# Optimization experiments

Hardware: AMD Instinct MI355X
Metric: run time of the kernel (lower is better)

Reference implementation:

```python
import jax, jax.numpy as jnp
import numpy as np

EPS = 1e-6

def oneplus(x):
    return 1.0 + jnp.log1p(jnp.exp(x) + EPS)

def content_addr(mem, keys, strength):
    # mem [B,N,M], keys [B,R,M], strength [B,R] -> [B,R,N]
    mn = jnp.sqrt(jnp.sum(mem * mem, -1))    # [B,N]
    kn = jnp.sqrt(jnp.sum(keys * keys, -1))  # [B,R]
    sim = jnp.einsum('brm,bnm->brn', keys, mem) / (kn[..., None] * mn[:, None, :] + EPS)
    return jax.nn.softmax(strength[..., None] * sim, axis=-1)

def setup_inputs() -> dict:
    key = jax.random.key(0)
    ks = jax.random.split(key, 16)
    B, T, W, R, N, M = 16, 32, 128, 4, 512, 128
    def lin(k, fi, fo):
        k1, k2 = jax.random.split(k)
        s = 1.0 / np.sqrt(fi)
        return (jax.random.uniform(k1, (fi, fo), minval=-s, maxval=s),
                jax.random.uniform(k2, (fo,), minval=-s, maxval=s))
    Din = W + R * W  # controller input: cat(x_t, prev_reads)
    Wb, bb = lin(ks[0], Din + W, W)     # CfC backbone (1 layer, silu)
    Wff1, bff1 = lin(ks[1], W, W)
    Wff2, bff2 = lin(ks[2], W, W)
    Wta, bta = lin(ks[3], W, W)
    Wtb, btb = lin(ks[4], W, W)
    Wv, bv = lin(ks[5], W, W)
    Wr, br = lin(ks[6], W * R, W)
    Wxi, bxi = lin(ks[7], W, W * R + 3 * W + 5 * R + 3)
    X = jax.random.normal(ks[8], (B, T, W), dtype=jnp.float32)
    hs = jnp.zeros((B, W), dtype=jnp.float32)
    mem = jax.random.normal(ks[9], (B, N, M), dtype=jnp.float32) * 0.1
    reset_idxs = jax.random.randint(ks[10], (B, T), 0, 2, dtype=jnp.int32)
    return {'X': X, 'hs': hs, 'mem': mem, 'reset_idxs': reset_idxs,
            'Wb': Wb, 'bb': bb, 'Wff1': Wff1, 'bff1': bff1, 'Wff2': Wff2, 'bff2': bff2,
            'Wta': Wta, 'bta': bta, 'Wtb': Wtb, 'btb': btb,
            'Wv': Wv, 'bv': bv, 'Wr': Wr, 'br': br, 'Wxi': Wxi, 'bxi': bxi}

def dnc_forward(X, hs, mem, reset_idxs, Wb, bb, Wff1, bff1, Wff2, bff2,
                Wta, bta, Wtb, btb, Wv, bv, Wr, br, Wxi, bxi):
    B, T, W = X.shape
    N, M = mem.shape[1], mem.shape[2]
    R = (bxi.shape[0] - 3 * W - 3) // (W + 5)
    eye = jnp.eye(N, dtype=mem.dtype)

    def step(carry, inp):
        hs, memv, prev_reads, prev_rw, prev_ww, usage, prec, link = carry
        x_t, reset, t = inp
        r = reset.astype(x_t.dtype)
        memv = memv * (1 - r)[:, None, None]   # memory.reset_idx
        hs = hs * (1 - r)[:, None]
        # CfC controller cell
        z = jax.nn.silu(jnp.concatenate([x_t, prev_reads, hs], -1) @ Wb + bb)
        ff1 = z @ Wff1 + bff1
        ff2 = z @ Wff2 + bff2
        ti = jax.nn.sigmoid((z @ Wta + bta) * t + (z @ Wtb + btb))
        hs = ff1 * (1 - ti) + ti * ff2
        # interface vector split
        xi = hs @ Wxi + bxi
        p = 0
        read_keys = xi[:, :W * R].reshape(B, R, W); p = W * R
        write_key = xi[:, p:p + W]; p += W
        write_vec = xi[:, p:p + W]; p += W
        erase = jax.nn.sigmoid(xi[:, p:p + W]); p += W
        free_g = jax.nn.sigmoid(xi[:, p:p + R]); p += R
        read_str = oneplus(xi[:, p:p + R]); p += R
        read_modes = jax.nn.softmax(xi[:, p:p + 3 * R].reshape(B, R, 3), -1); p += 3 * R
        write_str = oneplus(xi[:, p:p + 1]); p += 1
        alloc_g = jax.nn.sigmoid(xi[:, p:p + 1]); p += 1
        write_g = jax.nn.sigmoid(xi[:, p:p + 1])
        # write weights
        wca = content_addr(memv, write_key[:, None, :], write_str)[:, 0]  # [B,N]
        retention = jnp.prod(1 - free_g[:, :, None] * prev_rw, axis=1)
        usage = (usage + prev_ww - usage * prev_ww) * retention
        si = jnp.argsort(usage, -1)
        cp = jnp.cumprod(jnp.take_along_axis(usage, si, -1), -1)
        alloc = (1 - usage) * jnp.take_along_axis(cp, si, -1)  # gather(1, sorted_idx), as in source
        ww = write_g * (alloc_g * alloc + (1 - alloc_g) * wca)  # [B,N]
        wc = ww[:, :, None]
        link = (1 - wc - jnp.swapaxes(wc, 1, 2)) * link + wc * prec[:, None, :]
        link = link * (1 - eye)
        prec = (1 - ww.sum(-1, keepdims=True)) * prec + ww
        memv = memv * (1 - wc * erase[:, None, :]) + wc * write_vec[:, None, :]
        # read
        rca = content_addr(memv, read_keys, read_str)              # [B,R,N]
        fw = jnp.einsum('brn,bnk->brk', prev_rw, link)
        bw = jnp.einsum('brn,bkn->brk', prev_rw, link)
        aux = jnp.stack([bw, rca, fw], 2)                          # [B,R,3,N]
        rw = (aux * read_modes[..., None]).sum(2)
        reads = jnp.einsum('brn,bnm->brm', rw, memv).reshape(B, R * M)
        y = hs @ Wv + bv + reads @ Wr + br
        # prev_reads is detached each step in the source
        carry = (hs, memv, jax.lax.stop_gradient(reads), rw, ww, usage, prec, link)
        return carry, (y, hs)

    dt = X.dtype
    init = (hs, mem,
            jnp.zeros((B, R * W), dt), jnp.zeros((B, R, N), dt), jnp.zeros((B, N), dt),
            jnp.zeros((B, N), dt), jnp.zeros((B, N), dt), jnp.zeros((B, N, N), dt))
    xs = (jnp.swapaxes(X, 0, 1), jnp.swapaxes(reset_idxs, 0, 1), jnp.arange(T, dtype=dt))
    _, (ys, hss) = jax.lax.scan(step, init, xs)
    return jnp.swapaxes(ys, 0, 1), jnp.swapaxes(hss, 0, 1)

def reference(X, hs, mem, reset_idxs, Wb, bb, Wff1, bff1, Wff2, bff2,
              Wta, bta, Wtb, btb, Wv, bv, Wr, br, Wxi, bxi):
    return dnc_forward(X, hs, mem, reset_idxs, Wb, bb, Wff1, bff1, Wff2, bff2,
                       Wta, bta, Wtb, btb, Wv, bv, Wr, br, Wxi, bxi)
```

## Files before the change

kernel.cpp:

```cpp
#include <hip/hip_runtime.h>
#include <math.h>

#define Bq 16
#define Tq 32
#define Wq 128
#define Rq 4
#define Nq 512
#define Mq 128
#define DINq 768
#define XIDq 919
#define BTWq (Bq*Tq*Wq)

#define TSTRIDE 24576
#define TF_FW    0
#define TF_BW    16384
#define TF_RW    18432
#define TF_WW    20480
#define TF_PREC  20992
#define TF_XI    22016
#define TF_READS 23200
#define TF_CNT   23712

struct P {
  const float *X, *hs0, *mem0;
  const int *rst;
  const float *Wb,*bb,*Wff1,*bff1,*Wff2,*bff2,*Wta,*bta,*Wtb,*btb,*Wv,*bv,*Wr,*br,*Wxi,*bxi;
  float *out;
  float *rdh,*memv,*teams;
  float *WbT,*Wff1T,*Wff2T,*WtaT,*WtbT,*WvT,*WrT,*WxiT;
};

__device__ __forceinline__ float dot4(float4 a, float4 b){
  return a.x*b.x + a.y*b.y + a.z*b.z + a.w*b.w;
}
__device__ __forceinline__ float sigf(float x){ return 1.f/(1.f+expf(-x)); }
__device__ __forceinline__ float oneplusf(float x){ return 1.f + log1pf(expf(x) + 1e-6f); }

__device__ __forceinline__ void pst(float* p, float v){
  __hip_atomic_store(p, v, __ATOMIC_RELAXED, __HIP_MEMORY_SCOPE_AGENT);
}
__device__ __forceinline__ float pld(float* p){
  return __hip_atomic_load(p, __ATOMIC_RELAXED, __HIP_MEMORY_SCOPE_AGENT);
}
__device__ __forceinline__ void bump(unsigned* f){
  __syncthreads();
  if (threadIdx.x==0)
    __hip_atomic_fetch_add(f, 1u, __ATOMIC_RELAXED, __HIP_MEMORY_SCOPE_AGENT);
}
__device__ __forceinline__ void waitge(unsigned* f, unsigned v){
  if (threadIdx.x==0){
    while (__hip_atomic_fetch_add(f, 0u, __ATOMIC_RELAXED, __HIP_MEMORY_SCOPE_AGENT) < v)
      __builtin_amdgcn_s_sleep(1);
  }
  __syncthreads();
}

__device__ __forceinline__ float wave_sum64(float v){
  #pragma unroll
  for (int m=32;m>=1;m>>=1) v += __shfl_xor(v, m, 64);
  return v;
}
__device__ __forceinline__ float wave_max64(float v){
  #pragma unroll
  for (int m=32;m>=1;m>>=1) v = fmaxf(v, __shfl_xor(v, m, 64));
  return v;
}
__device__ __forceinline__ float blk_sum(float v, float* s8){
  int w = threadIdx.x>>6;
  v = wave_sum64(v);
  if ((threadIdx.x&63)==0) s8[w] = v;
  __syncthreads();
  float r = s8[0]+s8[1]+s8[2]+s8[3]+s8[4]+s8[5]+s8[6]+s8[7];
  __syncthreads();
  return r;
}
__device__ __forceinline__ float blk_max(float v, float* s8){
  int w = threadIdx.x>>6;
  v = wave_max64(v);
  if ((threadIdx.x&63)==0) s8[w] = v;
  __syncthreads();
  float r = s8[0];
  #pragma unroll
  for (int q=1;q<8;q++) r = fmaxf(r, s8[q]);
  __syncthreads();
  return r;
}

__global__ __launch_bounds__(256) void k_init(P p){
  int bid=blockIdx.x, tid=threadIdx.x;
  if (bid<8){ int idx=bid*256+tid, st=8*256;
    for (int k=idx;k<DINq*Wq;k+=st){ int j=k/DINq,i=k%DINq; p.WbT[k]=p.Wb[i*Wq+j]; }
  } else if (bid<10){ int idx=(bid-8)*256+tid, st=2*256;
    for (int k=idx;k<Wq*Wq;k+=st){ int j=k/Wq,i=k%Wq; p.Wff1T[k]=p.Wff1[i*Wq+j]; }
  } else if (bid<12){ int idx=(bid-10)*256+tid, st=2*256;
    for (int k=idx;k<Wq*Wq;k+=st){ int j=k/Wq,i=k%Wq; p.Wff2T[k]=p.Wff2[i*Wq+j]; }
  } else if (bid<14){ int idx=(bid-12)*256+tid, st=2*256;
    for (int k=idx;k<Wq*Wq;k+=st){ int j=k/Wq,i=k%Wq; p.WtaT[k]=p.Wta[i*Wq+j]; }
  } else if (bid<16){ int idx=(bid-14)*256+tid, st=2*256;
    for (int k=idx;k<Wq*Wq;k+=st){ int j=k/Wq,i=k%Wq; p.WtbT[k]=p.Wtb[i*Wq+j]; }
  } else if (bid<18){ int idx=(bid-16)*256+tid, st=2*256;
    for (int k=idx;k<Wq*Wq;k+=st){ int j=k/Wq,i=k%Wq; p.WvT[k]=p.Wv[i*Wq+j]; }
  } else if (bid<22){ int idx=(bid-18)*256+tid, st=4*256;
    for (int k=idx;k<Rq*Wq*Wq;k+=st){ int j=k/(Rq*Wq),i=k%(Rq*Wq); p.WrT[k]=p.Wr[i*Wq+j]; }
  } else if (bid<30){ int idx=(bid-22)*256+tid, st=8*256;
    for (int k=idx;k<XIDq*Wq;k+=st){ int f=k/Wq,i=k%Wq; p.WxiT[k]=p.Wxi[i*XIDq+f]; }
  } else if (bid<38){ int idx=(bid-30)*256+tid, st=8*256;
    for (int k=idx;k<16*TSTRIDE;k+=st) p.teams[k]=0.f;
  }
}

__global__ __launch_bounds__(512,2) void k_run(P p){
  const int tid=threadIdx.x, bid=blockIdx.x;
  const bool isA = (bid<16);
  const int team = isA ? bid : ((bid-16)>>3);
  const int g    = isA ? 0   : ((bid-16)&7);
  const int b=team;
  float* T = p.teams + (size_t)team*TSTRIDE;
  unsigned* C       = (unsigned*)(T + TF_CNT);
  unsigned* CNT_FW  = C + 0;
  unsigned* FLAG_RD = C + 32;
  unsigned* CNT_XI  = C + 64;
  unsigned* FLAG_WW = C + 96;

  __shared__ __align__(16) float inv[DINq];
  __shared__ __align__(16) float zl[Wq];
  __shared__ __align__(16) float hsl[Wq];
  __shared__ __align__(16) float acc4[4*Wq];
  __shared__ __align__(16) float rwl[Rq*Nq];
  __shared__ __align__(16) float rcl[Rq*Nq];
  __shared__ __align__(16) float key[Wq];
  __shared__ __align__(16) float keyv[Nq];
  __shared__ __align__(16) float xisc[32];
  __shared__ __align__(16) float wca[Nq];
  __shared__ __align__(16) float uarr[Nq];
  __shared__ __align__(16) float cpl[Nq];
  __shared__ __align__(16) float usage[Nq];
  __shared__ __align__(16) float wwl[Nq];
  __shared__ __align__(16) float precl[Nq];
  __shared__ __align__(16) float norms[Nq];
  __shared__ __align__(16) int   sidx[Nq];
  __shared__ __align__(16) float erl[Wq], wvl[Wq];
  __shared__ __align__(16) float fwacc[Rq*Nq];
  __shared__ float s8[8];

  if (isA){
    for (int i=tid;i<Nq*Mq/4;i+=512)
      ((float4*)(p.memv+(size_t)b*Nq*Mq))[i] = ((const float4*)(p.mem0+(size_t)b*Nq*Mq))[i];
    for (int i=tid;i<Rq*Nq;i+=512){ rwl[i]=0.f; rcl[i]=0.f; }
    usage[tid]=0.f; precl[tid]=0.f; wwl[tid]=0.f;
    inv[Wq+tid]=0.f;
    if (tid<Wq) hsl[tid]=p.hs0[b*Wq+tid];
    __syncthreads();
    { int n=tid;
      const float4* mr=(const float4*)(p.memv+((size_t)b*Nq+n)*Mq);
      float s=0.f;
      #pragma unroll 8
      for (int c=0;c<32;c++) s+=dot4(mr[c],mr[c]);
      norms[n]=sqrtf(s);
    }

    for (int t=0; t<=Tq; t++){
      if (t>0){
        waitge(CNT_FW, 8u*(unsigned)t);
        int n=tid;
        #pragma unroll
        for (int r=0;r<Rq;r++){
          float m0=xisc[8+r*3], m1=xisc[9+r*3], m2=xisc[10+r*3];
          float mm=fmaxf(m0,fmaxf(m1,m2));
          float e0=expf(m0-mm), e1=expf(m1-mm), e2=expf(m2-mm);
          float es=e0+e1+e2;
          float fwv=0.f;
          #pragma unroll
          for (int gg=0;gg<8;gg++) fwv += pld(T+TF_FW+gg*2048+r*Nq+n);
          float bwv = pld(T+TF_BW+r*Nq+n);
          float rwv = (e0*bwv + e1*rcl[r*Nq+n] + e2*fwv)/es;
          rwl[r*Nq+n]=rwv;
          pst(T+TF_RW+r*Nq+n, rwv);
        }
        __syncthreads();
        int p4=tid>>7, m=tid&127;
        const float* rr_ = rwl + p4*Nq;
        const float* mb = p.memv + (size_t)b*Nq*Mq + m;
        float a0=0.f,a1=0.f,a2=0.f,a3=0.f;
        for (int n2=0;n2<Nq;n2+=4){
          a0+=rr_[n2+0]*mb[(size_t)(n2+0)*Mq];
          a1+=rr_[n2+1]*mb[(size_t)(n2+1)*Mq];
          a2+=rr_[n2+2]*mb[(size_t)(n2+2)*Mq];
          a3+=rr_[n2+3]*mb[(size_t)(n2+3)*Mq];
        }
        float a=(a0+a1)+(a2+a3);
        inv[Wq+tid]=a;
        pst(T+TF_READS+tid, a);
        p.rdh[((size_t)b*Tq + (t-1))*Nq + tid] = a;
      }
      if (t==Tq) break;
      bump(FLAG_RD);

      float keep = 1.f - (float)p.rst[b*Tq + t];
      if (tid<Wq){
        inv[tid] = p.X[((size_t)b*Tq+t)*Wq + tid];
        inv[Wq+Nq+tid] = keep*hsl[tid];
      }
      __syncthreads();
      { int j=tid>>2, q=tid&3;
        const float4* w4=(const float4*)(p.WbT+(size_t)j*DINq);
        const float4* i4=(const float4*)inv;
        float a=0.f;
        for (int c=q;c<192;c+=4) a+=dot4(w4[c], i4[c]);
        a+=__shfl_xor(a,1,4); a+=__shfl_xor(a,2,4);
        if (q==0){ a+=p.bb[j]; zl[j]=a*sigf(a); }
      }
      __syncthreads();
      { int which=tid>>7, j=tid&127;
        const float* Wg=(which==0)?p.Wff1T:(which==1)?p.Wff2T:(which==2)?p.WtaT:p.WtbT;
        const float4* w4=(const float4*)(Wg+(size_t)j*Wq);
        const float4* z4=(const float4*)zl;
        float a=0.f;
        #pragma unroll 8
        for (int c=0;c<32;c++) a+=dot4(w4[c], z4[c]);
        acc4[which*Wq+j]=a;
      }
      __syncthreads();
      if (tid<Wq){
        float a1=acc4[tid]+p.bff1[tid], a2=acc4[Wq+tid]+p.bff2[tid];
        float aa=acc4[2*Wq+tid]+p.bta[tid], ab=acc4[3*Wq+tid]+p.btb[tid];
        float ti=sigf(aa*(float)t+ab);
        float h=a1*(1.f-ti)+ti*a2;
        hsl[tid]=h;
        p.out[BTWq + ((size_t)b*Tq+t)*Wq + tid]=h;
      }
      __syncthreads();
      if (tid<151){
        int f=(tid<Wq)? (512+tid) : (896+(tid-Wq));
        const float4* w4=(const float4*)(p.WxiT+(size_t)f*Wq);
        const float4* h4=(const float4*)hsl;
        float a=p.bxi[f];
        #pragma unroll 8
        for (int c=0;c<32;c++) a+=dot4(w4[c], h4[c]);
        if (tid<Wq) key[tid]=a; else xisc[tid-Wq]=a;
      }
      __syncthreads();
      {
        float kk2=(tid<Wq)? key[tid]*key[tid] : 0.f;
        float kn=sqrtf(blk_sum(kk2,s8));
        int n=tid;
        const float4* k4=(const float4*)key;
        const float4* mr=(const float4*)(p.memv+((size_t)b*Nq+n)*Mq);
        float d=0.f;
        #pragma unroll 8
        for (int c=0;c<32;c++) d+=dot4(k4[c],mr[c]);
        float mn=norms[n];
        float sim=(keep*d)/(kn*(keep*mn)+1e-6f);
        float wstr=oneplusf(xisc[20]);
        float v=wstr*sim;
        float mx=blk_max(v,s8);
        float e=expf(v-mx);
        float se=blk_sum(e,s8);
        wca[n]=e/se;
        float ret=1.f;
        #pragma unroll
        for (int r=0;r<Rq;r++) ret *= 1.f - sigf(xisc[r])*rwl[r*Nq+n];
        float uo=usage[n], pw=wwl[n];
        float u=(uo+pw-uo*pw)*ret;
        usage[n]=u; uarr[n]=u;
        __syncthreads();
        int rank=0;
        const float4* u4=(const float4*)uarr;
        #pragma unroll 8
        for (int jj=0;jj<128;jj++){
          float4 vv=u4[jj]; int j0=jj*4;
          rank += (vv.x<u)||(vv.x==u&&(j0+0)<n);
          rank += (vv.y<u)||(vv.y==u&&(j0+1)<n);
          rank += (vv.z<u)||(vv.z==u&&(j0+2)<n);
          rank += (vv.w<u)||(vv.w==u&&(j0+3)<n);
        }
        sidx[rank]=n;
        __syncthreads();
        int si=sidx[n];
        float sv=uarr[si];
        int w=tid>>6, l=tid&63;
        float x=sv;
        #pragma unroll
        for (int dd=1;dd<64;dd<<=1){
          float pr=__shfl_up(x,dd,64);
          if (l>=dd) x*=pr;
        }
        if (l==63) s8[w]=x;
        __syncthreads();
        float woff=1.f;
        #pragma unroll
        for (int q=0;q<8;q++) if (q<w) woff*=s8[q];
        x*=woff;
        cpl[n]=x;
        __syncthreads();
        float alloc=(1.f-u)*cpl[si];
        float ag=sigf(xisc[21]), wg=sigf(xisc[22]);
        float wwv=wg*(ag*alloc+(1.f-ag)*wca[n]);
        wwl[n]=wwv;
        pst(T+TF_WW+n, wwv);
        float wsum=blk_sum(wwv,s8);
        float pn=(1.f-wsum)*precl[n]+wwv;
        precl[n]=pn;
        pst(T+TF_PREC+(t&1)*Nq+n, pn);
      }
      bump(FLAG_WW);

      waitge(CNT_XI, 8u*(unsigned)(t+1));
      for (int i=tid;i<768;i+=512){
        if (i<512)      keyv[i]      = pld(T+TF_XI+i);
        else if (i<640) wvl[i-512]   = pld(T+TF_XI+128+i);
        else            erl[i-640]   = sigf(pld(T+TF_XI+128+i));
      }
      __syncthreads();
      {
        float kn4[Rq], rstr[Rq];
        #pragma unroll
        for (int r=0;r<Rq;r++){
          float kk2=(tid<Wq)? keyv[r*Wq+tid]*keyv[r*Wq+tid] : 0.f;
          kn4[r]=sqrtf(blk_sum(kk2,s8));
          rstr[r]=oneplusf(xisc[4+r]);
        }
        int n=tid;
        float wwn=wwl[n];
        float4* mrow=(float4*)(p.memv+((size_t)b*Nq+n)*Mq);
        const float4* er4=(const float4*)erl;
        const float4* wv4=(const float4*)wvl;
        const float4* k40=(const float4*)(keyv);
        const float4* k41=(const float4*)(keyv+128);
        const float4* k42=(const float4*)(keyv+256);
        const float4* k43=(const float4*)(keyv+384);
        float s=0.f,d0=0.f,d1=0.f,d2=0.f,d3=0.f;
        #pragma unroll 4
        for (int c=0;c<32;c++){
          float4 mv=mrow[c], e4=er4[c], w4=wv4[c];
          mv.x = mv.x*keep*(1.f-wwn*e4.x)+wwn*w4.x;
          mv.y = mv.y*keep*(1.f-wwn*e4.y)+wwn*w4.y;
          mv.z = mv.z*keep*(1.f-wwn*e4.z)+wwn*w4.z;
          mv.w = mv.w*keep*(1.f-wwn*e4.w)+wwn*w4.w;
          s+=dot4(mv,mv);
          d0+=dot4(k40[c],mv); d1+=dot4(k41[c],mv);
          d2+=dot4(k42[c],mv); d3+=dot4(k43[c],mv);
          mrow[c]=mv;
        }
        float mn=sqrtf(s);
        norms[n]=mn;
        float dd[4]={d0,d1,d2,d3};
        #pragma unroll
        for (int r=0;r<Rq;r++){
          float v=rstr[r]*(dd[r]/(kn4[r]*mn+1e-6f));
          float mx=blk_max(v,s8);
          float e=expf(v-mx);
          float se=blk_sum(e,s8);
          rcl[r*Nq+n]=e/se;
        }
      }
    }
  } else {
    float Lreg[8][8];
    #pragma unroll
    for (int rr=0;rr<8;rr++)
      #pragma unroll
      for (int q=0;q<8;q++) Lreg[rr][q]=0.f;
    if (tid<Wq) hsl[tid]=p.hs0[b*Wq+tid];
    __syncthreads();

    for (int t=0; t<Tq; t++){
      waitge(FLAG_RD, (unsigned)(t+1));
      float keep = 1.f - (float)p.rst[b*Tq + t];
      inv[Wq+tid] = pld(T+TF_READS+tid);
      if (tid<Wq){
        inv[tid] = p.X[((size_t)b*Tq+t)*Wq + tid];
        inv[Wq+Nq+tid] = keep*hsl[tid];
      }
      __syncthreads();
      { int j=tid>>2, q=tid&3;
        const float4* w4=(const float4*)(p.WbT+(size_t)j*DINq);
        const float4* i4=(const float4*)inv;
        float a=0.f;
        for (int c=q;c<192;c+=4) a+=dot4(w4[c], i4[c]);
        a+=__shfl_xor(a,1,4); a+=__shfl_xor(a,2,4);
        if (q==0){ a+=p.bb[j]; zl[j]=a*sigf(a); }
      }
      __syncthreads();
      { int which=tid>>7, j=tid&127;
        const float* Wg=(which==0)?p.Wff1T:(which==1)?p.Wff2T:(which==2)?p.WtaT:p.WtbT;
        const float4* w4=(const float4*)(Wg+(size_t)j*Wq);
        const float4* z4=(const float4*)zl;
        float a=0.f;
        #pragma unroll 8
        for (int c=0;c<32;c++) a+=dot4(w4[c], z4[c]);
        acc4[which*Wq+j]=a;
      }
      __syncthreads();
      if (tid<Wq){
        float a1=acc4[tid]+p.bff1[tid], a2=acc4[Wq+tid]+p.bff2[tid];
        float aa=acc4[2*Wq+tid]+p.bta[tid], ab=acc4[3*Wq+tid]+p.btb[tid];
        float ti=sigf(aa*(float)t+ab);
        hsl[tid]=a1*(1.f-ti)+ti*a2;
      }
      __syncthreads();
      { int rr=tid>>2, q=tid&3;
        if (rr<96){
          int idx=g*96+rr;
          int f=(idx<512)? idx : (idx+128);
          const float4* w4=(const float4*)(p.WxiT+(size_t)f*Wq);
          const float4* h4=(const float4*)hsl;
          float a=0.f;
          #pragma unroll
          for (int kk=0;kk<8;kk++) a+=dot4(w4[q*8+kk], h4[q*8+kk]);
          a+=__shfl_xor(a,1,4); a+=__shfl_xor(a,2,4);
          if (q==0) pst(T+TF_XI+f, a+p.bxi[f]);
        }
      }
      bump(CNT_XI);
      for (int i=tid;i<Rq*Nq;i+=512) rwl[i]=pld(T+TF_RW+i);
      precl[tid]=pld(T+TF_PREC+((t&1)^1)*Nq+tid);
      waitge(FLAG_WW, (unsigned)(t+1));
      wwl[tid]=pld(T+TF_WW+tid);
      for (int i=tid;i<Rq*Nq;i+=512) fwacc[i]=0.f;
      __syncthreads();
      { int w=tid>>6, l=tid&63, c0=l*8;
        float ww8[8], pc8[8], pr8[Rq][8];
        *(float4*)&ww8[0]=*(const float4*)&wwl[c0];   *(float4*)&ww8[4]=*(const float4*)&wwl[c0+4];
        *(float4*)&pc8[0]=*(const float4*)&precl[c0]; *(float4*)&pc8[4]=*(const float4*)&precl[c0+4];
        #pragma unroll
        for (int r=0;r<Rq;r++){
          *(float4*)&pr8[r][0]=*(const float4*)&rwl[r*Nq+c0];
          *(float4*)&pr8[r][4]=*(const float4*)&rwl[r*Nq+c0+4];
        }
        float fa[Rq][8];
        #pragma unroll
        for (int r=0;r<Rq;r++)
          #pragma unroll
          for (int q=0;q<8;q++) fa[r][q]=0.f;
        #pragma unroll
        for (int rr=0;rr<8;rr++){
          int n = g*64 + w*8 + rr;
          float wwn = wwl[n];
          float prn[Rq];
          #pragma unroll
          for (int r=0;r<Rq;r++) prn[r]=rwl[r*Nq+n];
          float bwp[Rq]={0.f,0.f,0.f,0.f};
          #pragma unroll
          for (int q=0;q<8;q++){
            float nv=(1.f-wwn-ww8[q])*Lreg[rr][q]+wwn*pc8[q];
            if (c0+q==n) nv=0.f;
            Lreg[rr][q]=nv;
            #pragma unroll
            for (int r=0;r<Rq;r++){ fa[r][q]+=prn[r]*nv; bwp[r]+=pr8[r][q]*nv; }
          }
          #pragma unroll
          for (int mm=1;mm<64;mm<<=1)
            #pragma unroll
            for (int r=0;r<Rq;r++) bwp[r]+=__shfl_xor(bwp[r],mm,64);
          if (l==0){
            #pragma unroll
            for (int r=0;r<Rq;r++) pst(T+TF_BW+r*Nq+n, bwp[r]);
          }
        }
        #pragma unroll
        for (int r=0;r<Rq;r++)
          #pragma unroll
          for (int q=0;q<8;q++) atomicAdd(&fwacc[r*Nq+c0+q], fa[r][q]);
        __syncthreads();
        for (int i=tid;i<Rq*Nq;i+=512) pst(T+TF_FW+g*2048+i, fwacc[i]);
      }
      bump(CNT_FW);
    }
  }
}

__global__ __launch_bounds__(512) void k_y(P p){
  int j=blockIdx.x, tid=threadIdx.x;
  __shared__ __align__(16) float wv[Wq];
  __shared__ __align__(16) float wr[Rq*Wq];
  if (tid<Wq) wv[tid]=p.WvT[(size_t)j*Wq+tid];
  wr[tid]=p.WrT[(size_t)j*(Rq*Wq)+tid];
  __syncthreads();
  int b=tid>>5, t=tid&31;
  const float4* h4=(const float4*)(p.out+BTWq+((size_t)b*Tq+t)*Wq);
  const float4* r4=(const float4*)(p.rdh+((size_t)b*Tq+t)*Nq);
  const float4* wv4=(const float4*)wv;
  const float4* wr4=(const float4*)wr;
  float a=0.f;
  #pragma unroll 8
  for (int c=0;c<32;c++) a+=dot4(wv4[c],h4[c]);
  #pragma unroll 8
  for (int c=0;c<128;c++) a+=dot4(wr4[c],r4[c]);
  p.out[((size_t)b*Tq+t)*Wq+j]=a+p.bv[j]+p.br[j];
}

extern "C" void kernel_launch(void* const* d_in, const int* in_sizes, int n_in,
                              void* d_out, int out_size, void* d_ws, size_t ws_size,
                              hipStream_t stream){
  (void)in_sizes; (void)n_in; (void)out_size; (void)ws_size;
  P p;
  p.X    = (const float*)d_in[0];
  p.hs0  = (const float*)d_in[1];
  p.mem0 = (const float*)d_in[2];
  p.rst  = (const int*)d_in[3];
  p.Wb   = (const float*)d_in[4];  p.bb   = (const float*)d_in[5];
  p.Wff1 = (const float*)d_in[6];  p.bff1 = (const float*)d_in[7];
  p.Wff2 = (const float*)d_in[8];  p.bff2 = (const float*)d_in[9];
  p.Wta  = (const float*)d_in[10]; p.bta  = (const float*)d_in[11];
  p.Wtb  = (const float*)d_in[12]; p.btb  = (const float*)d_in[13];
  p.Wv   = (const float*)d_in[14]; p.bv   = (const float*)d_in[15];
  p.Wr   = (const float*)d_in[16]; p.br   = (const float*)d_in[17];
  p.Wxi  = (const float*)d_in[18]; p.bxi  = (const float*)d_in[19];
  p.out  = (float*)d_out;
  float* ws = (float*)d_ws;
  size_t o = 0;
  p.rdh   = ws + o; o += (size_t)Bq*Tq*Nq;
  p.memv  = ws + o; o += (size_t)Bq*Nq*Mq;
  p.teams = ws + o; o += (size_t)16*TSTRIDE;
  p.WbT   = ws + o; o += (size_t)DINq*Wq;
  p.Wff1T = ws + o; o += (size_t)Wq*Wq;
  p.Wff2T = ws + o; o += (size_t)Wq*Wq;
  p.WtaT  = ws + o; o += (size_t)Wq*Wq;
  p.WtbT  = ws + o; o += (size_t)Wq*Wq;
  p.WvT   = ws + o; o += (size_t)Wq*Wq;
  p.WrT   = ws + o; o += (size_t)Rq*Wq*Wq;
  p.WxiT  = ws + o; o += (size_t)XIDq*Wq;

  hipLaunchKernelGGL(k_init, dim3(38),  dim3(256), 0, stream, p);
  hipLaunchKernelGGL(k_run,  dim3(144), dim3(512), 0, stream, p);
  hipLaunchKernelGGL(k_y,    dim3(128), dim3(512), 0, stream, p);
}
```

Baseline: 2.783 ms.

## Distribute memory matrix across 8 blocks per batch in registers, drop leader block

Removes the separate per-batch leader block that serially handled memory read, write and content addressing. Each batch is now handled by 8 symmetric blocks. Each block keeps its 64 rows of the memory matrix in registers, which removes the global memv buffer. Reads, write-content similarity and read-content scores are computed per block and combined through global partial buffers with counters. Every block redundantly computes the controller and the full xi projection, and the usage sort. The aim is to shorten the serial critical path per timestep, at the cost of extra cross-block barriers and duplicated controller work.

```diff
diff --git a/kernel.cpp b/kernel.cpp
--- a/kernel.cpp
+++ b/kernel.cpp
@@ -11,22 +11,20 @@
 #define XIDq 919
 #define BTWq (Bq*Tq*Wq)
 
-#define TSTRIDE 24576
+#define TSTRIDE 25600
 #define TF_FW    0
 #define TF_BW    16384
-#define TF_RW    18432
-#define TF_WW    20480
-#define TF_PREC  20992
-#define TF_XI    22016
-#define TF_READS 23200
-#define TF_CNT   23712
+#define TF_RCA   18432
+#define TF_PR    20480
+#define TF_WC    24576
+#define TF_CNT   25216
 
 struct P {
   const float *X, *hs0, *mem0;
   const int *rst;
   const float *Wb,*bb,*Wff1,*bff1,*Wff2,*bff2,*Wta,*bta,*Wtb,*btb,*Wv,*bv,*Wr,*br,*Wxi,*bxi;
   float *out;
-  float *rdh,*memv,*teams;
+  float *rdh,*teams;
   float *WbT,*Wff1T,*Wff2T,*WtaT,*WtbT,*WvT,*WrT,*WxiT;
 };
 
@@ -111,16 +109,18 @@
 
 __global__ __launch_bounds__(512,2) void k_run(P p){
   const int tid=threadIdx.x, bid=blockIdx.x;
-  const bool isA = (bid<16);
-  const int team = isA ? bid : ((bid-16)>>3);
-  const int g    = isA ? 0   : ((bid-16)&7);
-  const int b=team;
+  const int team=bid>>3, g=bid&7, b=team;
+  const int w=tid>>6, l=tid&63;
+  const int rg=l>>3, cg=l&7;
+  const int n_own = g*64 + w*8 + rg;
+  const int c0 = cg*16;
   float* T = p.teams + (size_t)team*TSTRIDE;
-  unsigned* C       = (unsigned*)(T + TF_CNT);
-  unsigned* CNT_FW  = C + 0;
-  unsigned* FLAG_RD = C + 32;
-  unsigned* CNT_XI  = C + 64;
-  unsigned* FLAG_WW = C + 96;
+  unsigned* C = (unsigned*)(T+TF_CNT);
+  unsigned* CNT_FW=C+0; unsigned* CNT_RD=C+32; unsigned* CNT_WC=C+64;
+
+  float4 m4[4];
+  float  nrm;
+  float  Lreg[8][8];
 
   __shared__ __align__(16) float inv[DINq];
   __shared__ __align__(16) float zl[Wq];
@@ -128,345 +128,305 @@
   __shared__ __align__(16) float acc4[4*Wq];
   __shared__ __align__(16) float rwl[Rq*Nq];
   __shared__ __align__(16) float rcl[Rq*Nq];
-  __shared__ __align__(16) float key[Wq];
-  __shared__ __align__(16) float keyv[Nq];
-  __shared__ __align__(16) float xisc[32];
-  __shared__ __align__(16) float wca[Nq];
-  __shared__ __align__(16) float uarr[Nq];
-  __shared__ __align__(16) float cpl[Nq];
+  __shared__ __align__(16) float fwacc[Rq*Nq];
+  __shared__ __align__(16) float scr2[2048];
+  __shared__ __align__(16) float xil[XIDq+9];
   __shared__ __align__(16) float usage[Nq];
   __shared__ __align__(16) float wwl[Nq];
   __shared__ __align__(16) float precl[Nq];
-  __shared__ __align__(16) float norms[Nq];
-  __shared__ __align__(16) int   sidx[Nq];
-  __shared__ __align__(16) float erl[Wq], wvl[Wq];
-  __shared__ __align__(16) float fwacc[Rq*Nq];
+  __shared__ __align__(16) float prl[Nq];
   __shared__ float s8[8];
 
-  if (isA){
-    for (int i=tid;i<Nq*Mq/4;i+=512)
-      ((float4*)(p.memv+(size_t)b*Nq*Mq))[i] = ((const float4*)(p.mem0+(size_t)b*Nq*Mq))[i];
-    for (int i=tid;i<Rq*Nq;i+=512){ rwl[i]=0.f; rcl[i]=0.f; }
-    usage[tid]=0.f; precl[tid]=0.f; wwl[tid]=0.f;
-    inv[Wq+tid]=0.f;
-    if (tid<Wq) hsl[tid]=p.hs0[b*Wq+tid];
-    __syncthreads();
-    { int n=tid;
-      const float4* mr=(const float4*)(p.memv+((size_t)b*Nq+n)*Mq);
-      float s=0.f;
-      #pragma unroll 8
-      for (int c=0;c<32;c++) s+=dot4(mr[c],mr[c]);
-      norms[n]=sqrtf(s);
-    }
-
-    for (int t=0; t<=Tq; t++){
-      if (t>0){
-        waitge(CNT_FW, 8u*(unsigned)t);
-        int n=tid;
-        #pragma unroll
-        for (int r=0;r<Rq;r++){
-          float m0=xisc[8+r*3], m1=xisc[9+r*3], m2=xisc[10+r*3];
-          float mm=fmaxf(m0,fmaxf(m1,m2));
-          float e0=expf(m0-mm), e1=expf(m1-mm), e2=expf(m2-mm);
-          float es=e0+e1+e2;
-          float fwv=0.f;
-          #pragma unroll
-          for (int gg=0;gg<8;gg++) fwv += pld(T+TF_FW+gg*2048+r*Nq+n);
-          float bwv = pld(T+TF_BW+r*Nq+n);
-          float rwv = (e0*bwv + e1*rcl[r*Nq+n] + e2*fwv)/es;
-          rwl[r*Nq+n]=rwv;
-          pst(T+TF_RW+r*Nq+n, rwv);
-        }
-        __syncthreads();
-        int p4=tid>>7, m=tid&127;
-        const float* rr_ = rwl + p4*Nq;
-        const float* mb = p.memv + (size_t)b*Nq*Mq + m;
-        float a0=0.f,a1=0.f,a2=0.f,a3=0.f;
-        for (int n2=0;n2<Nq;n2+=4){
-          a0+=rr_[n2+0]*mb[(size_t)(n2+0)*Mq];
-          a1+=rr_[n2+1]*mb[(size_t)(n2+1)*Mq];
-          a2+=rr_[n2+2]*mb[(size_t)(n2+2)*Mq];
-          a3+=rr_[n2+3]*mb[(size_t)(n2+3)*Mq];
-        }
-        float a=(a0+a1)+(a2+a3);
-        inv[Wq+tid]=a;
-        pst(T+TF_READS+tid, a);
-        p.rdh[((size_t)b*Tq + (t-1))*Nq + tid] = a;
-      }
-      if (t==Tq) break;
-      bump(FLAG_RD);
-
-      float keep = 1.f - (float)p.rst[b*Tq + t];
-      if (tid<Wq){
-        inv[tid] = p.X[((size_t)b*Tq+t)*Wq + tid];
-        inv[Wq+Nq+tid] = keep*hsl[tid];
-      }
-      __syncthreads();
-      { int j=tid>>2, q=tid&3;
-        const float4* w4=(const float4*)(p.WbT+(size_t)j*DINq);
-        const float4* i4=(const float4*)inv;
-        float a=0.f;
-        for (int c=q;c<192;c+=4) a+=dot4(w4[c], i4[c]);
-        a+=__shfl_xor(a,1,4); a+=__shfl_xor(a,2,4);
-        if (q==0){ a+=p.bb[j]; zl[j]=a*sigf(a); }
-      }
-      __syncthreads();
-      { int which=tid>>7, j=tid&127;
-        const float* Wg=(which==0)?p.Wff1T:(which==1)?p.Wff2T:(which==2)?p.WtaT:p.WtbT;
-        const float4* w4=(const float4*)(Wg+(size_t)j*Wq);
-        const float4* z4=(const float4*)zl;
-        float a=0.f;
-        #pragma unroll 8
-        for (int c=0;c<32;c++) a+=dot4(w4[c], z4[c]);
-        acc4[which*Wq+j]=a;
-      }
-      __syncthreads();
-      if (tid<Wq){
-        float a1=acc4[tid]+p.bff1[tid], a2=acc4[Wq+tid]+p.bff2[tid];
-        float aa=acc4[2*Wq+tid]+p.bta[tid], ab=acc4[3*Wq+tid]+p.btb[tid];
-        float ti=sigf(aa*(float)t+ab);
-        float h=a1*(1.f-ti)+ti*a2;
-        hsl[tid]=h;
-        p.out[BTWq + ((size_t)b*Tq+t)*Wq + tid]=h;
-      }
-      __syncthreads();
-      if (tid<151){
-        int f=(tid<Wq)? (512+tid) : (896+(tid-Wq));
-        const float4* w4=(const float4*)(p.WxiT+(size_t)f*Wq);
-        const float4* h4=(const float4*)hsl;
-        float a=p.bxi[f];
-        #pragma unroll 8
-        for (int c=0;c<32;c++) a+=dot4(w4[c], h4[c]);
-        if (tid<Wq) key[tid]=a; else xisc[tid-Wq]=a;
-      }
-      __syncthreads();
-      {
-        float kk2=(tid<Wq)? key[tid]*key[tid] : 0.f;
-        float kn=sqrtf(blk_sum(kk2,s8));
-        int n=tid;
-        const float4* k4=(const float4*)key;
-        const float4* mr=(const float4*)(p.memv+((size_t)b*Nq+n)*Mq);
-        float d=0.f;
-        #pragma unroll 8
-        for (int c=0;c<32;c++) d+=dot4(k4[c],mr[c]);
-        float mn=norms[n];
-        float sim=(keep*d)/(kn*(keep*mn)+1e-6f);
-        float wstr=oneplusf(xisc[20]);
-        float v=wstr*sim;
+  float* bwl  = scr2;
+  float* wcas = scr2;
+  float* uarr = scr2+512;
+  float* cpl  = scr2+1024;
+  int*   sidx = (int*)(scr2+1536);
+
+  { const float4* src=(const float4*)(p.mem0 + ((size_t)b*Nq+n_own)*Mq + c0);
+    float s=0.f;
+    #pragma unroll
+    for (int i=0;i<4;i++){ m4[i]=src[i]; s+=dot4(m4[i],m4[i]); }
+    s+=__shfl_xor(s,1,8); s+=__shfl_xor(s,2,8); s+=__shfl_xor(s,4,8);
+    nrm=sqrtf(s);
+  }
+  #pragma unroll
+  for (int rr=0;rr<8;rr++)
+    #pragma unroll
+    for (int q=0;q<8;q++) Lreg[rr][q]=0.f;
+  for (int i=tid;i<Rq*Nq;i+=512) rwl[i]=0.f;
+  usage[tid]=0.f; precl[tid]=0.f; wwl[tid]=0.f;
+  if (tid<Wq) hsl[tid]=p.hs0[b*Wq+tid];
+  __syncthreads();
+
+  for (int t=0; t<=Tq; t++){
+    if (t>0){
+      waitge(CNT_FW, 8u*(unsigned)t);
+      #pragma unroll
+      for (int k=0;k<4;k++){
+        int idx=tid+k*512;
+        float f0=pld(T+TF_FW+0*2048+idx), f1=pld(T+TF_FW+1*2048+idx);
+        float f2=pld(T+TF_FW+2*2048+idx), f3=pld(T+TF_FW+3*2048+idx);
+        float f4=pld(T+TF_FW+4*2048+idx), f5=pld(T+TF_FW+5*2048+idx);
+        float f6=pld(T+TF_FW+6*2048+idx), f7=pld(T+TF_FW+7*2048+idx);
+        fwacc[idx]=((f0+f1)+(f2+f3))+((f4+f5)+(f6+f7));
+        bwl[idx]=pld(T+TF_BW+idx);
+        rcl[idx]=pld(T+TF_RCA+idx);
+      }
+      __syncthreads();
+      #pragma unroll
+      for (int r=0;r<Rq;r++){
+        float v=rcl[r*Nq+tid];
         float mx=blk_max(v,s8);
         float e=expf(v-mx);
         float se=blk_sum(e,s8);
-        wca[n]=e/se;
-        float ret=1.f;
-        #pragma unroll
-        for (int r=0;r<Rq;r++) ret *= 1.f - sigf(xisc[r])*rwl[r*Nq+n];
-        float uo=usage[n], pw=wwl[n];
-        float u=(uo+pw-uo*pw)*ret;
-        usage[n]=u; uarr[n]=u;
-        __syncthreads();
-        int rank=0;
-        const float4* u4=(const float4*)uarr;
-        #pragma unroll 8
-        for (int jj=0;jj<128;jj++){
-          float4 vv=u4[jj]; int j0=jj*4;
-          rank += (vv.x<u)||(vv.x==u&&(j0+0)<n);
-          rank += (vv.y<u)||(vv.y==u&&(j0+1)<n);
-          rank += (vv.z<u)||(vv.z==u&&(j0+2)<n);
-          rank += (vv.w<u)||(vv.w==u&&(j0+3)<n);
-        }
-        sidx[rank]=n;
-        __syncthreads();
-        int si=sidx[n];
-        float sv=uarr[si];
-        int w=tid>>6, l=tid&63;
-        float x=sv;
-        #pragma unroll
-        for (int dd=1;dd<64;dd<<=1){
-          float pr=__shfl_up(x,dd,64);
-          if (l>=dd) x*=pr;
-        }
-        if (l==63) s8[w]=x;
-        __syncthreads();
-        float woff=1.f;
-        #pragma unroll
-        for (int q=0;q<8;q++) if (q<w) woff*=s8[q];
-        x*=woff;
-        cpl[n]=x;
-        __syncthreads();
-        float alloc=(1.f-u)*cpl[si];
-        float ag=sigf(xisc[21]), wg=sigf(xisc[22]);
-        float wwv=wg*(ag*alloc+(1.f-ag)*wca[n]);
-        wwl[n]=wwv;
-        pst(T+TF_WW+n, wwv);
-        float wsum=blk_sum(wwv,s8);
-        float pn=(1.f-wsum)*precl[n]+wwv;
-        precl[n]=pn;
-        pst(T+TF_PREC+(t&1)*Nq+n, pn);
-      }
-      bump(FLAG_WW);
-
-      waitge(CNT_XI, 8u*(unsigned)(t+1));
-      for (int i=tid;i<768;i+=512){
-        if (i<512)      keyv[i]      = pld(T+TF_XI+i);
-        else if (i<640) wvl[i-512]   = pld(T+TF_XI+128+i);
-        else            erl[i-640]   = sigf(pld(T+TF_XI+128+i));
-      }
-      __syncthreads();
-      {
-        float kn4[Rq], rstr[Rq];
-        #pragma unroll
-        for (int r=0;r<Rq;r++){
-          float kk2=(tid<Wq)? keyv[r*Wq+tid]*keyv[r*Wq+tid] : 0.f;
-          kn4[r]=sqrtf(blk_sum(kk2,s8));
-          rstr[r]=oneplusf(xisc[4+r]);
-        }
-        int n=tid;
-        float wwn=wwl[n];
-        float4* mrow=(float4*)(p.memv+((size_t)b*Nq+n)*Mq);
-        const float4* er4=(const float4*)erl;
-        const float4* wv4=(const float4*)wvl;
-        const float4* k40=(const float4*)(keyv);
-        const float4* k41=(const float4*)(keyv+128);
-        const float4* k42=(const float4*)(keyv+256);
-        const float4* k43=(const float4*)(keyv+384);
-        float s=0.f,d0=0.f,d1=0.f,d2=0.f,d3=0.f;
-        #pragma unroll 4
-        for (int c=0;c<32;c++){
-          float4 mv=mrow[c], e4=er4[c], w4=wv4[c];
-          mv.x = mv.x*keep*(1.f-wwn*e4.x)+wwn*w4.x;
-          mv.y = mv.y*keep*(1.f-wwn*e4.y)+wwn*w4.y;
-          mv.z = mv.z*keep*(1.f-wwn*e4.z)+wwn*w4.z;
-          mv.w = mv.w*keep*(1.f-wwn*e4.w)+wwn*w4.w;
-          s+=dot4(mv,mv);
-          d0+=dot4(k40[c],mv); d1+=dot4(k41[c],mv);
-          d2+=dot4(k42[c],mv); d3+=dot4(k43[c],mv);
-          mrow[c]=mv;
-        }
-        float mn=sqrtf(s);
-        norms[n]=mn;
-        float dd[4]={d0,d1,d2,d3};
-        #pragma unroll
-        for (int r=0;r<Rq;r++){
-          float v=rstr[r]*(dd[r]/(kn4[r]*mn+1e-6f));
-          float mx=blk_max(v,s8);
-          float e=expf(v-mx);
-          float se=blk_sum(e,s8);
-          rcl[r*Nq+n]=e/se;
-        }
-      }
-    }
-  } else {
-    float Lreg[8][8];
-    #pragma unroll
-    for (int rr=0;rr<8;rr++)
-      #pragma unroll
-      for (int q=0;q<8;q++) Lreg[rr][q]=0.f;
-    if (tid<Wq) hsl[tid]=p.hs0[b*Wq+tid];
-    __syncthreads();
-
-    for (int t=0; t<Tq; t++){
-      waitge(FLAG_RD, (unsigned)(t+1));
-      float keep = 1.f - (float)p.rst[b*Tq + t];
-      inv[Wq+tid] = pld(T+TF_READS+tid);
-      if (tid<Wq){
-        inv[tid] = p.X[((size_t)b*Tq+t)*Wq + tid];
-        inv[Wq+Nq+tid] = keep*hsl[tid];
-      }
-      __syncthreads();
-      { int j=tid>>2, q=tid&3;
-        const float4* w4=(const float4*)(p.WbT+(size_t)j*DINq);
-        const float4* i4=(const float4*)inv;
-        float a=0.f;
-        for (int c=q;c<192;c+=4) a+=dot4(w4[c], i4[c]);
-        a+=__shfl_xor(a,1,4); a+=__shfl_xor(a,2,4);
-        if (q==0){ a+=p.bb[j]; zl[j]=a*sigf(a); }
-      }
-      __syncthreads();
-      { int which=tid>>7, j=tid&127;
-        const float* Wg=(which==0)?p.Wff1T:(which==1)?p.Wff2T:(which==2)?p.WtaT:p.WtbT;
-        const float4* w4=(const float4*)(Wg+(size_t)j*Wq);
-        const float4* z4=(const float4*)zl;
-        float a=0.f;
-        #pragma unroll 8
-        for (int c=0;c<32;c++) a+=dot4(w4[c], z4[c]);
-        acc4[which*Wq+j]=a;
-      }
-      __syncthreads();
-      if (tid<Wq){
-        float a1=acc4[tid]+p.bff1[tid], a2=acc4[Wq+tid]+p.bff2[tid];
-        float aa=acc4[2*Wq+tid]+p.bta[tid], ab=acc4[3*Wq+tid]+p.btb[tid];
-        float ti=sigf(aa*(float)t+ab);
-        hsl[tid]=a1*(1.f-ti)+ti*a2;
-      }
-      __syncthreads();
-      { int rr=tid>>2, q=tid&3;
-        if (rr<96){
-          int idx=g*96+rr;
-          int f=(idx<512)? idx : (idx+128);
-          const float4* w4=(const float4*)(p.WxiT+(size_t)f*Wq);
-          const float4* h4=(const float4*)hsl;
-          float a=0.f;
-          #pragma unroll
-          for (int kk=0;kk<8;kk++) a+=dot4(w4[q*8+kk], h4[q*8+kk]);
-          a+=__shfl_xor(a,1,4); a+=__shfl_xor(a,2,4);
-          if (q==0) pst(T+TF_XI+f, a+p.bxi[f]);
-        }
-      }
-      bump(CNT_XI);
-      for (int i=tid;i<Rq*Nq;i+=512) rwl[i]=pld(T+TF_RW+i);
-      precl[tid]=pld(T+TF_PREC+((t&1)^1)*Nq+tid);
-      waitge(FLAG_WW, (unsigned)(t+1));
-      wwl[tid]=pld(T+TF_WW+tid);
-      for (int i=tid;i<Rq*Nq;i+=512) fwacc[i]=0.f;
-      __syncthreads();
-      { int w=tid>>6, l=tid&63, c0=l*8;
-        float ww8[8], pc8[8], pr8[Rq][8];
-        *(float4*)&ww8[0]=*(const float4*)&wwl[c0];   *(float4*)&ww8[4]=*(const float4*)&wwl[c0+4];
-        *(float4*)&pc8[0]=*(const float4*)&precl[c0]; *(float4*)&pc8[4]=*(const float4*)&precl[c0+4];
-        #pragma unroll
-        for (int r=0;r<Rq;r++){
-          *(float4*)&pr8[r][0]=*(const float4*)&rwl[r*Nq+c0];
-          *(float4*)&pr8[r][4]=*(const float4*)&rwl[r*Nq+c0+4];
-        }
-        float fa[Rq][8];
-        #pragma unroll
-        for (int r=0;r<Rq;r++)
-          #pragma unroll
-          for (int q=0;q<8;q++) fa[r][q]=0.f;
-        #pragma unroll
-        for (int rr=0;rr<8;rr++){
-          int n = g*64 + w*8 + rr;
-          float wwn = wwl[n];
-          float prn[Rq];
-          #pragma unroll
-          for (int r=0;r<Rq;r++) prn[r]=rwl[r*Nq+n];
-          float bwp[Rq]={0.f,0.f,0.f,0.f};
-          #pragma unroll
-          for (int q=0;q<8;q++){
-            float nv=(1.f-wwn-ww8[q])*Lreg[rr][q]+wwn*pc8[q];
-            if (c0+q==n) nv=0.f;
-            Lreg[rr][q]=nv;
-            #pragma unroll
-            for (int r=0;r<Rq;r++){ fa[r][q]+=prn[r]*nv; bwp[r]+=pr8[r][q]*nv; }
-          }
-          #pragma unroll
-          for (int mm=1;mm<64;mm<<=1)
-            #pragma unroll
-            for (int r=0;r<Rq;r++) bwp[r]+=__shfl_xor(bwp[r],mm,64);
-          if (l==0){
-            #pragma unroll
-            for (int r=0;r<Rq;r++) pst(T+TF_BW+r*Nq+n, bwp[r]);
+        rcl[r*Nq+tid]=e/se;
+      }
+      __syncthreads();
+      #pragma unroll
+      for (int k=0;k<4;k++){
+        int idx=tid+k*512, r=idx>>9;
+        float m0=xil[904+r*3],m1=xil[905+r*3],m2=xil[906+r*3];
+        float mm=fmaxf(m0,fmaxf(m1,m2));
+        float e0=expf(m0-mm),e1=expf(m1-mm),e2=expf(m2-mm);
+        float es=e0+e1+e2;
+        rwl[idx]=(e0*bwl[idx]+e1*rcl[idx]+e2*fwacc[idx])/es;
+      }
+      prl[tid]=0.f;
+      __syncthreads();
+      #pragma unroll
+      for (int r=0;r<Rq;r++){
+        float rwn=rwl[r*Nq+n_own];
+        #pragma unroll
+        for (int i=0;i<4;i++){
+          float ax=rwn*m4[i].x, ay=rwn*m4[i].y, az=rwn*m4[i].z, aw=rwn*m4[i].w;
+          ax+=__shfl_xor(ax,8,64); ax+=__shfl_xor(ax,16,64); ax+=__shfl_xor(ax,32,64);
+          ay+=__shfl_xor(ay,8,64); ay+=__shfl_xor(ay,16,64); ay+=__shfl_xor(ay,32,64);
+          az+=__shfl_xor(az,8,64); az+=__shfl_xor(az,16,64); az+=__shfl_xor(az,32,64);
+          aw+=__shfl_xor(aw,8,64); aw+=__shfl_xor(aw,16,64); aw+=__shfl_xor(aw,32,64);
+          if (rg==0){
+            atomicAdd(&prl[r*Wq+c0+i*4+0],ax);
+            atomicAdd(&prl[r*Wq+c0+i*4+1],ay);
+            atomicAdd(&prl[r*Wq+c0+i*4+2],az);
+            atomicAdd(&prl[r*Wq+c0+i*4+3],aw);
           }
         }
-        #pragma unroll
-        for (int r=0;r<Rq;r++)
+      }
+      __syncthreads();
+      pst(T+TF_PR+g*512+tid, prl[tid]);
+      bump(CNT_RD);
+      waitge(CNT_RD, 8u*(unsigned)t);
+      { float s=0.f;
+        #pragma unroll
+        for (int gg=0;gg<8;gg++) s+=pld(T+TF_PR+gg*512+tid);
+        inv[Wq+tid]=s;
+        if (g==0) p.rdh[((size_t)b*Tq+(t-1))*Nq+tid]=s;
+      }
+      __syncthreads();
+    } else {
+      inv[Wq+tid]=0.f;
+      __syncthreads();
+    }
+    if (t==Tq) break;
+
+    float keep = 1.f - (float)p.rst[b*Tq + t];
+    if (tid<Wq){
+      inv[tid]=p.X[((size_t)b*Tq+t)*Wq+tid];
+      inv[Wq+Nq+tid]=keep*hsl[tid];
+    }
+    __syncthreads();
+    { int j=tid>>2,q=tid&3;
+      const float4* w4=(const float4*)(p.WbT+(size_t)j*DINq);
+      const float4* i4=(const float4*)inv;
+      float a=0.f;
+      for (int c=q;c<192;c+=4) a+=dot4(w4[c],i4[c]);
+      a+=__shfl_xor(a,1,4); a+=__shfl_xor(a,2,4);
+      if (q==0){ a+=p.bb[j]; zl[j]=a*sigf(a); }
+    }
+    __syncthreads();
+    { int which=tid>>7,j=tid&127;
+      const float* Wg=(which==0)?p.Wff1T:(which==1)?p.Wff2T:(which==2)?p.WtaT:p.WtbT;
+      const float4* w4=(const float4*)(Wg+(size_t)j*Wq);
+      const float4* z4=(const float4*)zl;
+      float a=0.f;
+      #pragma unroll 8
+      for (int c=0;c<32;c++) a+=dot4(w4[c],z4[c]);
+      acc4[which*Wq+j]=a;
+    }
+    __syncthreads();
+    if (tid<Wq){
+      float a1=acc4[tid]+p.bff1[tid], a2=acc4[Wq+tid]+p.bff2[tid];
+      float aa=acc4[2*Wq+tid]+p.bta[tid], ab=acc4[3*Wq+tid]+p.btb[tid];
+      float ti=sigf(aa*(float)t+ab);
+      float h=a1*(1.f-ti)+ti*a2;
+      hsl[tid]=h;
+      if (g==0) p.out[BTWq+((size_t)b*Tq+t)*Wq+tid]=h;
+    }
+    __syncthreads();
+    { const float4* h4=(const float4*)hsl;
+      int f=tid;
+      { const float4* w4=(const float4*)(p.WxiT+(size_t)f*Wq);
+        float a=p.bxi[f];
+        #pragma unroll 8
+        for (int c=0;c<32;c++) a+=dot4(w4[c],h4[c]);
+        xil[f]=a;
+      }
+      int f2=tid+512;
+      if (f2<XIDq){
+        const float4* w4=(const float4*)(p.WxiT+(size_t)f2*Wq);
+        float a=p.bxi[f2];
+        #pragma unroll 8
+        for (int c=0;c<32;c++) a+=dot4(w4[c],h4[c]);
+        xil[f2]=a;
+      }
+    }
+    __syncthreads();
+    { float kk=(tid<Wq)? xil[512+tid]*xil[512+tid]:0.f;
+      float kn=sqrtf(blk_sum(kk,s8));
+      const float4* k4=(const float4*)(xil+512);
+      float d=0.f;
+      #pragma unroll
+      for (int i=0;i<4;i++) d+=dot4(k4[cg*4+i],m4[i]);
+      d+=__shfl_xor(d,1,8); d+=__shfl_xor(d,2,8); d+=__shfl_xor(d,4,8);
+      float wstr=oneplusf(xil[916]);
+      float sim=(keep*d)/(kn*(keep*nrm)+1e-6f);
+      if (cg==0) pst(T+TF_WC+n_own, wstr*sim);
+    }
+    bump(CNT_WC);
+    waitge(CNT_WC, 8u*(unsigned)(t+1));
+    { float v=pld(T+TF_WC+tid);
+      float mx=blk_max(v,s8);
+      float e=expf(v-mx);
+      float se=blk_sum(e,s8);
+      wcas[tid]=e/se;
+    }
+    __syncthreads();
+    float wsum;
+    { int n=tid;
+      float ret=1.f;
+      #pragma unroll
+      for (int r=0;r<Rq;r++) ret *= 1.f - sigf(xil[896+r])*rwl[r*Nq+n];
+      float uo=usage[n], pw=wwl[n];
+      float u=(uo+pw-uo*pw)*ret;
+      usage[n]=u; uarr[n]=u;
+      __syncthreads();
+      int rank=0;
+      const float4* u4=(const float4*)uarr;
+      #pragma unroll 8
+      for (int jj=0;jj<128;jj++){
+        float4 vv=u4[jj]; int j0=jj*4;
+        rank += (vv.x<u)||(vv.x==u&&(j0+0)<n);
+        rank += (vv.y<u)||(vv.y==u&&(j0+1)<n);
+        rank += (vv.z<u)||(vv.z==u&&(j0+2)<n);
+        rank += (vv.w<u)||(vv.w==u&&(j0+3)<n);
+      }
+      sidx[rank]=n;
+      __syncthreads();
+      int si=sidx[n];
+      float sv=uarr[si];
+      float x=sv;
+      #pragma unroll
+      for (int dd=1;dd<64;dd<<=1){
+        float pr=__shfl_up(x,dd,64);
+        if (l>=dd) x*=pr;
+      }
+      if (l==63) s8[w]=x;
+      __syncthreads();
+      float woff=1.f;
+      #pragma unroll
+      for (int q=0;q<8;q++) if (q<w) woff*=s8[q];
+      x*=woff;
+      cpl[n]=x;
+      __syncthreads();
+      float alloc=(1.f-u)*cpl[si];
+      float ag=sigf(xil[917]), wg=sigf(xil[918]);
+      float wwv=wg*(ag*alloc+(1.f-ag)*wcas[n]);
+      wwl[n]=wwv;
+      wsum=blk_sum(wwv,s8);
+    }
+    { for (int i=tid;i<Rq*Nq;i+=512) fwacc[i]=0.f;
+      __syncthreads();
+      int c0p=l*8;
+      float ww8[8], pc8[8], pr8[Rq][8];
+      *(float4*)&ww8[0]=*(const float4*)&wwl[c0p];   *(float4*)&ww8[4]=*(const float4*)&wwl[c0p+4];
+      *(float4*)&pc8[0]=*(const float4*)&precl[c0p]; *(float4*)&pc8[4]=*(const float4*)&precl[c0p+4];
+      #pragma unroll
+      for (int r=0;r<Rq;r++){
+        *(float4*)&pr8[r][0]=*(const float4*)&rwl[r*Nq+c0p];
+        *(float4*)&pr8[r][4]=*(const float4*)&rwl[r*Nq+c0p+4];
+      }
+      float fa[Rq][8];
+      #pragma unroll
+      for (int r=0;r<Rq;r++)
+        #pragma unroll
+        for (int q=0;q<8;q++) fa[r][q]=0.f;
+      #pragma unroll
+      for (int rr=0;rr<8;rr++){
+        int n = g*64 + w*8 + rr;
+        float wwn = wwl[n];
+        float prn[Rq];
+        #pragma unroll
+        for (int r=0;r<Rq;r++) prn[r]=rwl[r*Nq+n];
+        float bwp[Rq]={0.f,0.f,0.f,0.f};
+        #pragma unroll
+        for (int q=0;q<8;q++){
+          float nv=(1.f-wwn-ww8[q])*Lreg[rr][q]+wwn*pc8[q];
+          if (c0p+q==n) nv=0.f;
+          Lreg[rr][q]=nv;
           #pragma unroll
-          for (int q=0;q<8;q++) atomicAdd(&fwacc[r*Nq+c0+q], fa[r][q]);
-        __syncthreads();
-        for (int i=tid;i<Rq*Nq;i+=512) pst(T+TF_FW+g*2048+i, fwacc[i]);
-      }
-      bump(CNT_FW);
-    }
+          for (int r=0;r<Rq;r++){ fa[r][q]+=prn[r]*nv; bwp[r]+=pr8[r][q]*nv; }
+        }
+        #pragma unroll
+        for (int mm=1;mm<64;mm<<=1)
+          #pragma unroll
+          for (int r=0;r<Rq;r++) bwp[r]+=__shfl_xor(bwp[r],mm,64);
+        if (l==0){
+          #pragma unroll
+          for (int r=0;r<Rq;r++) pst(T+TF_BW+r*Nq+n, bwp[r]);
+        }
+      }
+      #pragma unroll
+      for (int r=0;r<Rq;r++)
+        #pragma unroll
+        for (int q=0;q<8;q++) atomicAdd(&fwacc[r*Nq+c0p+q], fa[r][q]);
+      __syncthreads();
+      for (int i=tid;i<Rq*Nq;i+=512) pst(T+TF_FW+g*2048+i, fwacc[i]);
+    }
+    precl[tid]=(1.f-wsum)*precl[tid]+wwl[tid];
+    __syncthreads();
+    { float wwn=wwl[n_own];
+      float s=0.f;
+      #pragma unroll
+      for (int i=0;i<4;i++){
+        float e0=sigf(xil[768+c0+i*4+0]), e1=sigf(xil[768+c0+i*4+1]);
+        float e2=sigf(xil[768+c0+i*4+2]), e3=sigf(xil[768+c0+i*4+3]);
+        m4[i].x = m4[i].x*keep*(1.f-wwn*e0) + wwn*xil[640+c0+i*4+0];
+        m4[i].y = m4[i].y*keep*(1.f-wwn*e1) + wwn*xil[640+c0+i*4+1];
+        m4[i].z = m4[i].z*keep*(1.f-wwn*e2) + wwn*xil[640+c0+i*4+2];
+        m4[i].w = m4[i].w*keep*(1.f-wwn*e3) + wwn*xil[640+c0+i*4+3];
+        s+=dot4(m4[i],m4[i]);
+      }
+      s+=__shfl_xor(s,1,8); s+=__shfl_xor(s,2,8); s+=__shfl_xor(s,4,8);
+      nrm=sqrtf(s);
+      float kn4[Rq], rstr[Rq];
+      #pragma unroll
+      for (int r=0;r<Rq;r++){
+        float kk=(tid<Wq)? xil[r*Wq+tid]*xil[r*Wq+tid]:0.f;
+        kn4[r]=sqrtf(blk_sum(kk,s8));
+        rstr[r]=oneplusf(xil[900+r]);
+      }
+      #pragma unroll
+      for (int r=0;r<Rq;r++){
+        const float4* kr=(const float4*)(xil+r*Wq);
+        float d=0.f;
+        #pragma unroll
+        for (int i=0;i<4;i++) d+=dot4(kr[cg*4+i],m4[i]);
+        d+=__shfl_xor(d,1,8); d+=__shfl_xor(d,2,8); d+=__shfl_xor(d,4,8);
+        float v=rstr[r]*(d/(kn4[r]*nrm+1e-6f));
+        if (cg==0) pst(T+TF_RCA+r*Nq+n_own, v);
+      }
+    }
+    bump(CNT_FW);
   }
 }
 
@@ -511,7 +471,6 @@
   float* ws = (float*)d_ws;
   size_t o = 0;
   p.rdh   = ws + o; o += (size_t)Bq*Tq*Nq;
-  p.memv  = ws + o; o += (size_t)Bq*Nq*Mq;
   p.teams = ws + o; o += (size_t)16*TSTRIDE;
   p.WbT   = ws + o; o += (size_t)DINq*Wq;
   p.Wff1T = ws + o; o += (size_t)Wq*Wq;
@@ -523,6 +482,6 @@
   p.WxiT  = ws + o; o += (size_t)XIDq*Wq;
 
   hipLaunchKernelGGL(k_init, dim3(38),  dim3(256), 0, stream, p);
-  hipLaunchKernelGGL(k_run,  dim3(144), dim3(512), 0, stream, p);
+  hipLaunchKernelGGL(k_run,  dim3(128), dim3(512), 0, stream, p);
   hipLaunchKernelGGL(k_y,    dim3(128), dim3(512), 0, stream, p);
 }
```

Measured after the change: 3.780 ms. +35.8%, slower.
